# Optimization experiments

Hardware: AMD Instinct MI355X
Metric: run time of the kernel (lower is better)

Reference implementation:

```python
import jax, jax.numpy as jnp
import numpy as np

C = 80          # NUM_CLASSES
D = 8525        # total anchors over FPN levels (640 input: 80^2+40^2+20^2+10^2+5^2)
B = 64
EPS = 1e-6


def setup_inputs() -> dict:
    key = jax.random.key(0)
    ks = jax.random.split(key, 8)
    outs = jax.random.normal(ks[0], (B, D, C + 5), dtype=jnp.float32)
    grids = jax.random.uniform(ks[1], (D, 2), dtype=jnp.float32) * 640.0  # anchor centers (px)
    # --- build gres = [gcls(C), centerness(1), g_ltrb(4), mask_pp(1), mask_pos(1), pad(1)] ---
    labels = jax.random.randint(ks[2], (B, D), 0, C)
    mask_pos = (jax.random.uniform(ks[3], (B, D)) < 0.10).astype(jnp.float32)  # in-box positives
    mask_pp = (jax.random.uniform(ks[4], (B, D)) < 0.05).astype(jnp.float32)   # center-radius positives
    gcls = jax.nn.one_hot(labels, C, dtype=jnp.float32) * mask_pos[..., None]
    gcenterness = jax.random.uniform(ks[5], (B, D), dtype=jnp.float32)
    off = jax.random.uniform(ks[6], (B, D, 4), dtype=jnp.float32) * 64.0 + 1.0
    gx = grids[None, :, 0]
    gy = grids[None, :, 1]
    g_ltrb = jnp.stack([gx - off[..., 0], gy - off[..., 1],
                        gx + off[..., 2], gy + off[..., 3]], axis=-1)
    gres = jnp.concatenate([gcls,
                            gcenterness[..., None],
                            g_ltrb,
                            mask_pp[..., None],
                            mask_pos[..., None],
                            jnp.zeros((B, D, 1), jnp.float32)], axis=-1)  # [B, D, 88]
    nums_pos = jax.random.randint(ks[7], (B,), 1, 21).astype(jnp.int32)
    return {"outs": outs, "gres": gres, "grids": grids, "nums_pos": nums_pos}


def _giou(p, g):
    # elementwise GIoU on ltrb boxes, p/g: [..., 4]
    ix1 = jnp.maximum(p[..., 0], g[..., 0]); iy1 = jnp.maximum(p[..., 1], g[..., 1])
    ix2 = jnp.minimum(p[..., 2], g[..., 2]); iy2 = jnp.minimum(p[..., 3], g[..., 3])
    inter = jnp.clip(ix2 - ix1, 0.0) * jnp.clip(iy2 - iy1, 0.0)
    area_p = jnp.clip(p[..., 2] - p[..., 0], 0.0) * jnp.clip(p[..., 3] - p[..., 1], 0.0)
    area_g = jnp.clip(g[..., 2] - g[..., 0], 0.0) * jnp.clip(g[..., 3] - g[..., 1], 0.0)
    union = area_p + area_g - inter
    iou = inter / (union + EPS)
    cx1 = jnp.minimum(p[..., 0], g[..., 0]); cy1 = jnp.minimum(p[..., 1], g[..., 1])
    cx2 = jnp.maximum(p[..., 2], g[..., 2]); cy2 = jnp.maximum(p[..., 3], g[..., 3])
    c_area = (cx2 - cx1) * (cy2 - cy1)
    return iou - (c_area - union) / (c_area + EPS)


def reference(outs, gres, grids, nums_pos):
    np_f = nums_pos.astype(jnp.float32)
    # ---- cls: focal loss over all anchors ----
    pcls = jax.nn.sigmoid(outs[..., :C])          # [B, D, C]
    gcls = gres[..., :C]
    pos_m = (gcls == 1.0).astype(pcls.dtype)
    l_pos = -0.25 * (1.0 - pcls) ** 2 * jnp.log(pcls + EPS) * pos_m
    l_neg = -0.75 * pcls ** 2 * jnp.log(1.0 - pcls + EPS) * (1.0 - pos_m)
    l_cls_pos = jnp.mean(jnp.sum(l_pos, axis=(1, 2)) / np_f)
    l_cls_neg = jnp.mean(jnp.sum(l_neg, axis=(1, 2)) / np_f)
    # ---- conf: BCE(pconf, 1) over center-radius positives ----
    mask_pp = (gres[..., C + 5] == 1.0).astype(outs.dtype)
    pconf = jax.nn.sigmoid(outs[..., C])
    bce = -jnp.log(pconf + EPS)                    # target = ones
    l_conf = 5.0 * jnp.mean(jnp.sum(bce * mask_pp, axis=-1) / np_f)
    # ---- reg: masked GIoU over in-box positives ----
    mask_pos = (gres[..., C + 6] == 1.0).astype(outs.dtype)
    poff = outs[..., C + 1:C + 5]
    gxy = grids[None]                              # [1, D, 2]
    pboxes = jnp.concatenate([gxy - poff[..., :2], gxy + poff[..., 2:]], axis=-1)
    g_ltrb = gres[..., C + 1:C + 5]
    giou = _giou(pboxes, g_ltrb)                   # [B, D]
    gcenter = gres[..., C]
    n_pos = jnp.maximum(jnp.sum(mask_pos), 1.0)
    l_reg = 5.0 * jnp.sum((1.0 - giou) * gcenter * mask_pos) / n_pos
    return l_cls_pos + l_cls_neg + l_conf + l_reg
```

## Files before the change

kernel.cpp:

```cpp
#include <hip/hip_runtime.h>

namespace {

constexpr int   kC    = 80;
constexpr int   kD    = 8525;
constexpr int   kB    = 64;
constexpr float kEps  = 1e-6f;
constexpr int   kOC   = 85;
constexpr int   kGC   = 88;
constexpr int   kBlk  = 256;
constexpr int   kPB   = kD * kOC;
constexpr int   kSpb  = 32;
constexpr int   kRPS  = (kD + kSpb - 1) / kSpb;
constexpr int   kNT   = kB * kSpb;

__device__ __forceinline__ float wave_reduce(float v) {
#pragma unroll
  for (int o = 32; o > 0; o >>= 1) v += __shfl_down(v, o, 64);
  return v;
}

__device__ __forceinline__ float fast_rcp(float x) {
  return __builtin_amdgcn_rcpf(x);
}

__device__ __forceinline__ float lneg_raw(float x) {
  const float t = __expf(-x);
  const float p = fast_rcp(1.0f + t);
  return p * p * __logf(1.0f - p + kEps);
}

__global__ __launch_bounds__(kBlk) void floss_fused(
    const float* __restrict__ outs, const float* __restrict__ gres,
    const float* __restrict__ grids, const int* __restrict__ nums_pos,
    float* __restrict__ partials) {
  const int bid = blockIdx.x;
  const int tid = threadIdx.x;
  const int b   = bid >> 5;
  const int sb  = bid & 31;
  const int r0  = sb * kRPS;
  const int r1  = (r0 + kRPS < kD) ? r0 + kRPS : kD;
  const float scale = fast_rcp(64.0f * (float)nums_pos[b]);

  float pm = 0.f, pr = 0.f, pn = 0.f;

  {
    const int gA = b * kPB + r0 * kOC;
    const int gB = b * kPB + r1 * kOC;
    const int gv = (gA + 3) & ~3;
    const int nvec = (gB - gv) >> 2;
    const int gvend = gv + (nvec << 2);
    float a0 = 0.f, a1 = 0.f, a2 = 0.f, a3 = 0.f;
    if (tid < gv - gA)    a0 += lneg_raw(outs[gA + tid]);
    if (tid < gB - gvend) a1 += lneg_raw(outs[gvend + tid]);
#pragma unroll 2
    for (int v = tid; v < nvec; v += kBlk) {
      const float4 x = *(const float4*)(outs + gv + 4 * v);
      a0 += lneg_raw(x.x);
      a1 += lneg_raw(x.y);
      a2 += lneg_raw(x.z);
      a3 += lneg_raw(x.w);
    }
    pm += -0.75f * scale * ((a0 + a1) + (a2 + a3));
  }

  for (int r = r0 + tid; r < r1; r += kBlk) {
    const int row = b * kD + r;
    const float* orow = outs + (size_t)row * kOC;
    const float x80 = orow[80], x81 = orow[81], x82 = orow[82],
                x83 = orow[83], x84 = orow[84];
    const float t5 = ((lneg_raw(x80) + lneg_raw(x81)) +
                      (lneg_raw(x82) + lneg_raw(x83))) + lneg_raw(x84);
    pm += 0.75f * scale * t5;

    const size_t gbase = (size_t)row * kGC;
    const float4 t0 = *(const float4*)(gres + gbase + 80);
    const float4 t1 = *(const float4*)(gres + gbase + 84);

    if (t1.y == 1.0f) {
      const float pc = fast_rcp(1.0f + __expf(-x80));
      pm += -5.0f * __logf(pc + kEps) * scale;
    }
    if (t1.z == 1.0f) {
      pn += 1.0f;
      int lab = 0;
      const float4* gc = (const float4*)(gres + gbase);
#pragma unroll 5
      for (int j = 0; j < 20; ++j) {
        const float4 v = gc[j];
        if (v.x == 1.0f) lab = 4 * j;
        if (v.y == 1.0f) lab = 4 * j + 1;
        if (v.z == 1.0f) lab = 4 * j + 2;
        if (v.w == 1.0f) lab = 4 * j + 3;
      }
      const float x = orow[lab];
      const float t = __expf(-x);
      const float p = fast_rcp(1.0f + t);
      const float om = 1.0f - p;
      const float lp = -0.25f * om * om * __logf(p + kEps);
      const float ln = -0.75f * p * p * __logf(om + kEps);
      pm += (lp - ln) * scale;
      const float gx = grids[2 * r + 0];
      const float gy = grids[2 * r + 1];
      const float p0 = gx - x81, p1 = gy - x82;
      const float p2 = gx + x83, p3 = gy + x84;
      const float g0 = t0.y, g1 = t0.z, g2 = t0.w, g3 = t1.x;
      const float iw = fmaxf(fminf(p2, g2) - fmaxf(p0, g0), 0.f);
      const float ih = fmaxf(fminf(p3, g3) - fmaxf(p1, g1), 0.f);
      const float inter = iw * ih;
      const float ap = fmaxf(p2 - p0, 0.f) * fmaxf(p3 - p1, 0.f);
      const float ag = fmaxf(g2 - g0, 0.f) * fmaxf(g3 - g1, 0.f);
      const float un = ap + ag - inter;
      const float iou = inter * fast_rcp(un + kEps);
      const float ca = (fmaxf(p2, g2) - fminf(p0, g0)) *
                       (fmaxf(p3, g3) - fminf(p1, g1));
      const float giou = iou - (ca - un) * fast_rcp(ca + kEps);
      pr += (1.0f - giou) * t0.x;
    }
  }

  __shared__ float sm[3][kBlk / 64];
  const float vm = wave_reduce(pm);
  const float vr = wave_reduce(pr);
  const float vn = wave_reduce(pn);
  const int lane = tid & 63;
  const int w    = tid >> 6;
  if (lane == 0) { sm[0][w] = vm; sm[1][w] = vr; sm[2][w] = vn; }
  __syncthreads();
  if (tid == 0) {
    float m = 0.f, r = 0.f, n = 0.f;
#pragma unroll
    for (int j = 0; j < kBlk / 64; ++j) { m += sm[0][j]; r += sm[1][j]; n += sm[2][j]; }
    partials[bid * 3 + 0] = m;
    partials[bid * 3 + 1] = r;
    partials[bid * 3 + 2] = n;
  }
}

__global__ __launch_bounds__(kBlk) void floss_final(
    const float* __restrict__ partials, float* __restrict__ out) {
  float m = 0.f, r = 0.f, n = 0.f;
  for (int i = threadIdx.x; i < kNT; i += kBlk) {
    m += partials[i * 3 + 0];
    r += partials[i * 3 + 1];
    n += partials[i * 3 + 2];
  }
  __shared__ float sm[3][kBlk / 64];
  m = wave_reduce(m); r = wave_reduce(r); n = wave_reduce(n);
  const int lane = threadIdx.x & 63;
  const int w    = threadIdx.x >> 6;
  if (lane == 0) { sm[0][w] = m; sm[1][w] = r; sm[2][w] = n; }
  __syncthreads();
  if (threadIdx.x == 0) {
    float tm = 0.f, tr = 0.f, tn = 0.f;
#pragma unroll
    for (int j = 0; j < kBlk / 64; ++j) { tm += sm[0][j]; tr += sm[1][j]; tn += sm[2][j]; }
    out[0] = tm + 5.0f * tr / fmaxf(tn, 1.0f);
  }
}

}

extern "C" void kernel_launch(void* const* d_in, const int* in_sizes, int n_in,
                              void* d_out, int out_size, void* d_ws, size_t ws_size,
                              hipStream_t stream) {
  const float* outs     = (const float*)d_in[0];
  const float* gres     = (const float*)d_in[1];
  const float* grids    = (const float*)d_in[2];
  const int*   nums_pos = (const int*)d_in[3];
  float* partials = (float*)d_ws;

  floss_fused<<<kNT, kBlk, 0, stream>>>(outs, gres, grids, nums_pos, partials);
  floss_final<<<1, kBlk, 0, stream>>>(partials, (float*)d_out);
}
```

Measured before the change: 67.06 us.

## Stage row tails in LDS and cooperatively gather positive-anchor labels per wave

The streaming pass now computes a column index for each element, so it evaluates the negative focal term only on the 80 class logits and writes the five conf/box values into shared memory instead of computing and later cancelling them. Positive anchors are handled wave-cooperatively: a ballot over positives lets the whole wave load the 88-wide gres row in parallel and find the label with a second ballot, rather than each thread scanning 80 floats serially. Grids are staged in LDS, and launch bounds request higher occupancy. The cost is a per-element divide by 85, extra branches, and a serialized per-positive loop in which only lane 0 computes the loss.

```diff
diff --git a/kernel.cpp b/kernel.cpp
--- a/kernel.cpp
+++ b/kernel.cpp
@@ -25,12 +25,11 @@
 }
 
 __device__ __forceinline__ float lneg_raw(float x) {
-  const float t = __expf(-x);
-  const float p = fast_rcp(1.0f + t);
+  const float p = fast_rcp(1.0f + __expf(-x));
   return p * p * __logf(1.0f - p + kEps);
 }
 
-__global__ __launch_bounds__(kBlk) void floss_fused(
+__global__ __launch_bounds__(kBlk, 8) void floss_fused(
     const float* __restrict__ outs, const float* __restrict__ gres,
     const float* __restrict__ grids, const int* __restrict__ nums_pos,
     float* __restrict__ partials) {
@@ -40,91 +39,117 @@
   const int sb  = bid & 31;
   const int r0  = sb * kRPS;
   const int r1  = (r0 + kRPS < kD) ? r0 + kRPS : kD;
+  const int nrows = r1 - r0;
   const float scale = fast_rcp(64.0f * (float)nums_pos[b]);
 
+  __shared__ float s_tail[kRPS * 5];
+  __shared__ float s_grids[kRPS * 2];
+  __shared__ float sm[3][kBlk / 64];
+
+  for (int i = tid; i < 2 * nrows; i += kBlk) s_grids[i] = grids[2 * r0 + i];
+
   float pm = 0.f, pr = 0.f, pn = 0.f;
 
   {
-    const int gA = b * kPB + r0 * kOC;
-    const int gB = b * kPB + r1 * kOC;
-    const int gv = (gA + 3) & ~3;
+    const int sliceStart = b * kPB + r0 * kOC;
+    const int gB = sliceStart + nrows * kOC;
+    const int gv = (sliceStart + 3) & ~3;
     const int nvec = (gB - gv) >> 2;
     const int gvend = gv + (nvec << 2);
-    float a0 = 0.f, a1 = 0.f, a2 = 0.f, a3 = 0.f;
-    if (tid < gv - gA)    a0 += lneg_raw(outs[gA + tid]);
-    if (tid < gB - gvend) a1 += lneg_raw(outs[gvend + tid]);
-#pragma unroll 2
-    for (int v = tid; v < nvec; v += kBlk) {
-      const float4 x = *(const float4*)(outs + gv + 4 * v);
-      a0 += lneg_raw(x.x);
-      a1 += lneg_raw(x.y);
-      a2 += lneg_raw(x.z);
-      a3 += lneg_raw(x.w);
-    }
-    pm += -0.75f * scale * ((a0 + a1) + (a2 + a3));
-  }
-
-  for (int r = r0 + tid; r < r1; r += kBlk) {
-    const int row = b * kD + r;
-    const float* orow = outs + (size_t)row * kOC;
-    const float x80 = orow[80], x81 = orow[81], x82 = orow[82],
-                x83 = orow[83], x84 = orow[84];
-    const float t5 = ((lneg_raw(x80) + lneg_raw(x81)) +
-                      (lneg_raw(x82) + lneg_raw(x83))) + lneg_raw(x84);
-    pm += 0.75f * scale * t5;
-
-    const size_t gbase = (size_t)row * kGC;
-    const float4 t0 = *(const float4*)(gres + gbase + 80);
-    const float4 t1 = *(const float4*)(gres + gbase + 84);
-
-    if (t1.y == 1.0f) {
-      const float pc = fast_rcp(1.0f + __expf(-x80));
-      pm += -5.0f * __logf(pc + kEps) * scale;
-    }
-    if (t1.z == 1.0f) {
-      pn += 1.0f;
-      int lab = 0;
-      const float4* gc = (const float4*)(gres + gbase);
-#pragma unroll 5
-      for (int j = 0; j < 20; ++j) {
-        const float4 v = gc[j];
-        if (v.x == 1.0f) lab = 4 * j;
-        if (v.y == 1.0f) lab = 4 * j + 1;
-        if (v.z == 1.0f) lab = 4 * j + 2;
-        if (v.w == 1.0f) lab = 4 * j + 3;
+    float lacc = 0.f;
+    if (tid < gv - sliceStart) lacc += lneg_raw(outs[sliceStart + tid]);
+    if (tid < gB - gvend) {
+      const unsigned off = (unsigned)(gvend - sliceStart) + tid;
+      const float x = outs[gvend + tid];
+      const unsigned rl = off / 85u;
+      const unsigned c  = off - 85u * rl;
+      if (c < 80u) lacc += lneg_raw(x);
+      else         s_tail[rl * 5 + (c - 80u)] = x;
+    }
+    for (int g = gv + 4 * tid; g < gvend; g += 4 * kBlk) {
+      const float4 xv = *(const float4*)(outs + g);
+      const unsigned off = (unsigned)(g - sliceStart);
+      const unsigned rl = off / 85u;
+      const unsigned c  = off - 85u * rl;
+      const float xs[4] = {xv.x, xv.y, xv.z, xv.w};
+#pragma unroll
+      for (int k2 = 0; k2 < 4; ++k2) {
+        unsigned ck = c + k2, rk = rl;
+        if (ck >= 85u) { ck -= 85u; rk += 1u; }
+        if (ck < 80u) lacc += lneg_raw(xs[k2]);
+        else          s_tail[rk * 5 + (ck - 80u)] = xs[k2];
       }
-      const float x = orow[lab];
-      const float t = __expf(-x);
-      const float p = fast_rcp(1.0f + t);
-      const float om = 1.0f - p;
-      const float lp = -0.25f * om * om * __logf(p + kEps);
-      const float ln = -0.75f * p * p * __logf(om + kEps);
-      pm += (lp - ln) * scale;
-      const float gx = grids[2 * r + 0];
-      const float gy = grids[2 * r + 1];
-      const float p0 = gx - x81, p1 = gy - x82;
-      const float p2 = gx + x83, p3 = gy + x84;
-      const float g0 = t0.y, g1 = t0.z, g2 = t0.w, g3 = t1.x;
-      const float iw = fmaxf(fminf(p2, g2) - fmaxf(p0, g0), 0.f);
-      const float ih = fmaxf(fminf(p3, g3) - fmaxf(p1, g1), 0.f);
-      const float inter = iw * ih;
-      const float ap = fmaxf(p2 - p0, 0.f) * fmaxf(p3 - p1, 0.f);
-      const float ag = fmaxf(g2 - g0, 0.f) * fmaxf(g3 - g1, 0.f);
-      const float un = ap + ag - inter;
-      const float iou = inter * fast_rcp(un + kEps);
-      const float ca = (fmaxf(p2, g2) - fminf(p0, g0)) *
-                       (fmaxf(p3, g3) - fminf(p1, g1));
-      const float giou = iou - (ca - un) * fast_rcp(ca + kEps);
-      pr += (1.0f - giou) * t0.x;
-    }
-  }
-
-  __shared__ float sm[3][kBlk / 64];
+    }
+    pm += -0.75f * scale * lacc;
+  }
+  __syncthreads();
+
+  const int w    = tid >> 6;
+  const int lane = tid & 63;
+  for (int k = 0; k < 2; ++k) {
+    const int rl = k * kBlk + tid;
+    const bool valid = rl < nrows;
+    float4 t0 = make_float4(0.f, 0.f, 0.f, 0.f), t1 = t0;
+    bool pos = false;
+    if (valid) {
+      const size_t gb = (size_t)(b * kD + r0 + rl) * kGC;
+      t0 = *(const float4*)(gres + gb + 80);
+      t1 = *(const float4*)(gres + gb + 84);
+      if (t1.y == 1.0f) {
+        const float pc = fast_rcp(1.0f + __expf(-s_tail[rl * 5]));
+        pm += -5.0f * __logf(pc + kEps) * scale;
+      }
+      pos = (t1.z == 1.0f);
+      if (pos) pn += 1.f;
+    }
+    unsigned long long mask = __ballot(pos);
+    while (mask) {
+      const int j = (int)(__ffsll((unsigned long long)mask) - 1);
+      mask &= mask - 1;
+      const int prl = k * kBlk + (w << 6) + j;
+      const float gcen = __shfl(t0.x, j);
+      const float g0   = __shfl(t0.y, j);
+      const float g1   = __shfl(t0.z, j);
+      const float g2   = __shfl(t0.w, j);
+      const float g3   = __shfl(t1.x, j);
+      const size_t gb2 = (size_t)(b * kD + r0 + prl) * kGC;
+      const float gv1 = gres[gb2 + lane];
+      const float gv2 = (lane < 16) ? gres[gb2 + 64 + lane] : 0.f;
+      const unsigned long long m1 = __ballot(gv1 == 1.0f);
+      const unsigned long long m2 = __ballot((lane < 16) && gv2 == 1.0f);
+      if ((m1 | m2) == 0ull) continue;
+      const int lab = m1 ? (int)(__ffsll(m1) - 1) : 64 + (int)(__ffsll(m2) - 1);
+      if (lane == 0) {
+        const size_t ob = (size_t)(b * kD + r0 + prl) * kOC;
+        const float x  = outs[ob + lab];
+        const float p  = fast_rcp(1.0f + __expf(-x));
+        const float om = 1.0f - p;
+        const float lp = -0.25f * om * om * __logf(p + kEps);
+        const float ln = -0.75f * p * p * __logf(om + kEps);
+        pm += (lp - ln) * scale;
+        const float x81 = s_tail[prl * 5 + 1], x82 = s_tail[prl * 5 + 2];
+        const float x83 = s_tail[prl * 5 + 3], x84 = s_tail[prl * 5 + 4];
+        const float gx = s_grids[2 * prl], gy = s_grids[2 * prl + 1];
+        const float p0 = gx - x81, p1 = gy - x82;
+        const float p2 = gx + x83, p3 = gy + x84;
+        const float iw = fmaxf(fminf(p2, g2) - fmaxf(p0, g0), 0.f);
+        const float ih = fmaxf(fminf(p3, g3) - fmaxf(p1, g1), 0.f);
+        const float inter = iw * ih;
+        const float ap = fmaxf(p2 - p0, 0.f) * fmaxf(p3 - p1, 0.f);
+        const float ag = fmaxf(g2 - g0, 0.f) * fmaxf(g3 - g1, 0.f);
+        const float un = ap + ag - inter;
+        const float iou = inter * fast_rcp(un + kEps);
+        const float ca = (fmaxf(p2, g2) - fminf(p0, g0)) *
+                         (fmaxf(p3, g3) - fminf(p1, g1));
+        const float giou = iou - (ca - un) * fast_rcp(ca + kEps);
+        pr += (1.0f - giou) * gcen;
+      }
+    }
+  }
+
   const float vm = wave_reduce(pm);
   const float vr = wave_reduce(pr);
   const float vn = wave_reduce(pn);
-  const int lane = tid & 63;
-  const int w    = tid >> 6;
   if (lane == 0) { sm[0][w] = vm; sm[1][w] = vr; sm[2][w] = vn; }
   __syncthreads();
   if (tid == 0) {
```

After: 73.01 us. 1.09x slower.

## Queue positive anchors in shared memory and search labels cooperatively across lanes

Applied to the files above, without the earlier changes.

Positive rows are no longer handled inline, where one thread serially scanned 20 float4s of the one-hot class vector under divergence. Each positive row is now appended to a shared-memory queue via a shared atomic. A second phase has 32 lanes per queued entry each load one float4 of the one-hot vector, find the label with a max-shuffle reduction, and let lane 0 compute the focal and GIoU terms. The dense streaming loop is also unrolled to four independent float4 loads per iteration, and launch bounds request 8 blocks per CU. The trade-off is about 13 KB of shared memory per block and two extra barriers, plus a re-read of gres rows in the second phase.

```diff
diff --git a/kernel.cpp b/kernel.cpp
--- a/kernel.cpp
+++ b/kernel.cpp
@@ -13,6 +13,7 @@
 constexpr int   kSpb  = 32;
 constexpr int   kRPS  = (kD + kSpb - 1) / kSpb;
 constexpr int   kNT   = kB * kSpb;
+constexpr int   kQW   = 12;
 
 __device__ __forceinline__ float wave_reduce(float v) {
 #pragma unroll
@@ -25,12 +26,15 @@
 }
 
 __device__ __forceinline__ float lneg_raw(float x) {
-  const float t = __expf(-x);
-  const float p = fast_rcp(1.0f + t);
+  const float p = fast_rcp(1.0f + __expf(-x));
   return p * p * __logf(1.0f - p + kEps);
 }
 
-__global__ __launch_bounds__(kBlk) void floss_fused(
+__device__ __forceinline__ float lneg4(const float4 v) {
+  return (lneg_raw(v.x) + lneg_raw(v.y)) + (lneg_raw(v.z) + lneg_raw(v.w));
+}
+
+__global__ __launch_bounds__(kBlk, 8) void floss_fused(
     const float* __restrict__ outs, const float* __restrict__ gres,
     const float* __restrict__ grids, const int* __restrict__ nums_pos,
     float* __restrict__ partials) {
@@ -40,86 +44,118 @@
   const int sb  = bid & 31;
   const int r0  = sb * kRPS;
   const int r1  = (r0 + kRPS < kD) ? r0 + kRPS : kD;
+  const int nrows = r1 - r0;
   const float scale = fast_rcp(64.0f * (float)nums_pos[b]);
+
+  __shared__ float s_q[kRPS * kQW];
+  __shared__ int   s_cnt;
+  __shared__ float sm[3][kBlk / 64];
+  if (tid == 0) s_cnt = 0;
 
   float pm = 0.f, pr = 0.f, pn = 0.f;
 
   {
     const int gA = b * kPB + r0 * kOC;
-    const int gB = b * kPB + r1 * kOC;
+    const int gB = gA + nrows * kOC;
     const int gv = (gA + 3) & ~3;
     const int nvec = (gB - gv) >> 2;
     const int gvend = gv + (nvec << 2);
     float a0 = 0.f, a1 = 0.f, a2 = 0.f, a3 = 0.f;
     if (tid < gv - gA)    a0 += lneg_raw(outs[gA + tid]);
     if (tid < gB - gvend) a1 += lneg_raw(outs[gvend + tid]);
-#pragma unroll 2
-    for (int v = tid; v < nvec; v += kBlk) {
-      const float4 x = *(const float4*)(outs + gv + 4 * v);
-      a0 += lneg_raw(x.x);
-      a1 += lneg_raw(x.y);
-      a2 += lneg_raw(x.z);
-      a3 += lneg_raw(x.w);
-    }
+    const float* pv = outs + gv;
+    int v = tid;
+    for (; v + 3 * kBlk < nvec; v += 4 * kBlk) {
+      const float4 xa = *(const float4*)(pv + 4 * v);
+      const float4 xb = *(const float4*)(pv + 4 * (v + kBlk));
+      const float4 xc = *(const float4*)(pv + 4 * (v + 2 * kBlk));
+      const float4 xd = *(const float4*)(pv + 4 * (v + 3 * kBlk));
+      a0 += lneg4(xa);
+      a1 += lneg4(xb);
+      a2 += lneg4(xc);
+      a3 += lneg4(xd);
+    }
+    for (; v < nvec; v += kBlk) a0 += lneg4(*(const float4*)(pv + 4 * v));
     pm += -0.75f * scale * ((a0 + a1) + (a2 + a3));
   }
-
-  for (int r = r0 + tid; r < r1; r += kBlk) {
+  __syncthreads();
+
+  for (int rl = tid; rl < nrows; rl += kBlk) {
+    const int r   = r0 + rl;
     const int row = b * kD + r;
     const float* orow = outs + (size_t)row * kOC;
     const float x80 = orow[80], x81 = orow[81], x82 = orow[82],
                 x83 = orow[83], x84 = orow[84];
+    const size_t gb = (size_t)row * kGC;
+    const float4 t0 = *(const float4*)(gres + gb + 80);
+    const float4 t1 = *(const float4*)(gres + gb + 84);
     const float t5 = ((lneg_raw(x80) + lneg_raw(x81)) +
-                      (lneg_raw(x82) + lneg_raw(x83))) + lneg_raw(x84);
+                     (lneg_raw(x82) + lneg_raw(x83))) + lneg_raw(x84);
     pm += 0.75f * scale * t5;
-
-    const size_t gbase = (size_t)row * kGC;
-    const float4 t0 = *(const float4*)(gres + gbase + 80);
-    const float4 t1 = *(const float4*)(gres + gbase + 84);
-
     if (t1.y == 1.0f) {
       const float pc = fast_rcp(1.0f + __expf(-x80));
       pm += -5.0f * __logf(pc + kEps) * scale;
     }
     if (t1.z == 1.0f) {
       pn += 1.0f;
-      int lab = 0;
-      const float4* gc = (const float4*)(gres + gbase);
-#pragma unroll 5
-      for (int j = 0; j < 20; ++j) {
-        const float4 v = gc[j];
-        if (v.x == 1.0f) lab = 4 * j;
-        if (v.y == 1.0f) lab = 4 * j + 1;
-        if (v.z == 1.0f) lab = 4 * j + 2;
-        if (v.w == 1.0f) lab = 4 * j + 3;
+      const int slot = atomicAdd(&s_cnt, 1);
+      float* q = s_q + slot * kQW;
+      q[0]  = t0.x;
+      q[1]  = t0.y; q[2] = t0.z; q[3] = t0.w; q[4] = t1.x;
+      q[5]  = x81;  q[6] = x82;  q[7] = x83;  q[8] = x84;
+      q[9]  = grids[2 * r + 0];
+      q[10] = grids[2 * r + 1];
+      q[11] = __int_as_float(row);
+    }
+  }
+  __syncthreads();
+
+  {
+    const int nq = s_cnt;
+    const int hh = tid >> 5;
+    const int h  = tid & 31;
+    for (int e = hh; e < nq; e += 8) {
+      const float* q = s_q + e * kQW;
+      const int row = __float_as_int(q[11]);
+      int cand = -1;
+      if (h < 20) {
+        const float4 v = *(const float4*)(gres + (size_t)row * kGC + 4 * h);
+        if (v.x == 1.0f) cand = 4 * h;
+        if (v.y == 1.0f) cand = 4 * h + 1;
+        if (v.z == 1.0f) cand = 4 * h + 2;
+        if (v.w == 1.0f) cand = 4 * h + 3;
       }
-      const float x = orow[lab];
-      const float t = __expf(-x);
-      const float p = fast_rcp(1.0f + t);
-      const float om = 1.0f - p;
-      const float lp = -0.25f * om * om * __logf(p + kEps);
-      const float ln = -0.75f * p * p * __logf(om + kEps);
-      pm += (lp - ln) * scale;
-      const float gx = grids[2 * r + 0];
-      const float gy = grids[2 * r + 1];
-      const float p0 = gx - x81, p1 = gy - x82;
-      const float p2 = gx + x83, p3 = gy + x84;
-      const float g0 = t0.y, g1 = t0.z, g2 = t0.w, g3 = t1.x;
-      const float iw = fmaxf(fminf(p2, g2) - fmaxf(p0, g0), 0.f);
-      const float ih = fmaxf(fminf(p3, g3) - fmaxf(p1, g1), 0.f);
-      const float inter = iw * ih;
-      const float ap = fmaxf(p2 - p0, 0.f) * fmaxf(p3 - p1, 0.f);
-      const float ag = fmaxf(g2 - g0, 0.f) * fmaxf(g3 - g1, 0.f);
-      const float un = ap + ag - inter;
-      const float iou = inter * fast_rcp(un + kEps);
-      const float ca = (fmaxf(p2, g2) - fminf(p0, g0)) *
-                       (fmaxf(p3, g3) - fminf(p1, g1));
-      const float giou = iou - (ca - un) * fast_rcp(ca + kEps);
-      pr += (1.0f - giou) * t0.x;
-    }
-  }
-
-  __shared__ float sm[3][kBlk / 64];
+#pragma unroll
+      for (int m = 16; m > 0; m >>= 1) {
+        const int o = __shfl_xor(cand, m, 32);
+        cand = (o > cand) ? o : cand;
+      }
+      if (h == 0 && cand >= 0) {
+        const float x  = outs[(size_t)row * kOC + cand];
+        const float p  = fast_rcp(1.0f + __expf(-x));
+        const float om = 1.0f - p;
+        const float lp = -0.25f * om * om * __logf(p + kEps);
+        const float ln = -0.75f * p * p * __logf(om + kEps);
+        pm += (lp - ln) * scale;
+        const float gx = q[9], gy = q[10];
+        const float p0 = gx - q[5], p1 = gy - q[6];
+        const float p2 = gx + q[7], p3 = gy + q[8];
+        const float g0 = q[1], g1 = q[2], g2 = q[3], g3 = q[4];
+        const float iw = fmaxf(fminf(p2, g2) - fmaxf(p0, g0), 0.f);
+        const float ih = fmaxf(fminf(p3, g3) - fmaxf(p1, g1), 0.f);
+        const float inter = iw * ih;
+        const float ap = fmaxf(p2 - p0, 0.f) * fmaxf(p3 - p1, 0.f);
+        const float ag = fmaxf(g2 - g0, 0.f) * fmaxf(g3 - g1, 0.f);
+        const float un = ap + ag - inter;
+        const float iou = inter * fast_rcp(un + kEps);
+        const float ca = (fmaxf(p2, g2) - fminf(p0, g0)) *
+                         (fmaxf(p3, g3) - fminf(p1, g1));
+        const float giou = iou - (ca - un) * fast_rcp(ca + kEps);
+        pr += (1.0f - giou) * q[0];
+      }
+    }
+  }
+
   const float vm = wave_reduce(pm);
   const float vr = wave_reduce(pr);
   const float vn = wave_reduce(pn);
```

Measured after the change: 64.31 us. 4.1% less time.
